# Kernel optimization log

Measured on AMD Instinct MI355X. Metric: run time of the kernel, lower is better.

## Reference

```python
import jax, jax.numpy as jnp
import numpy as np

M, K, N = 8192, 4096, 4096
ALPHA, BETA = 0.002, 0.0005


def setup_inputs() -> dict:
    key = jax.random.key(0)
    kx, kw, kb = jax.random.split(key, 3)
    # int8-range quantized activations and weights (stored as int32 for portability)
    x = jax.random.randint(kx, (M, K), -127, 127, dtype=jnp.int32)
    weight = jax.random.randint(kw, (N, K), -127, 127, dtype=jnp.int32)  # (out, in)
    bias = jax.random.randint(kb, (1, N), -(2**20), 2**20, dtype=jnp.int32)
    alpha = jnp.float32(ALPHA)
    beta = jnp.float32(BETA)
    return {"x": x, "weight": weight, "bias": bias, "alpha": alpha, "beta": beta}


def reference(x, weight, bias, alpha, beta):
    # int8 GEMM with int32 accumulation: acc[m, n] = sum_k x[m, k] * W[n, k]
    acc = jnp.matmul(x, weight.T, preferred_element_type=jnp.int32)  # [M, N] int32
    # CUTLASS-style epilogue: D = round(alpha * acc + beta * bias) -> int32
    y = alpha * acc.astype(jnp.float32) + beta * bias.astype(jnp.float32)
    return jnp.round(y).astype(jnp.int32)
```

## Files before the change

### kernel.cpp

```cpp
#include <hip/hip_runtime.h>
#include <hip/hip_bf16.h>
#include <stdint.h>

#define M_DIM 8192
#define N_DIM 4096
#define K_DIM 4096

#define BM 256
#define BN 256
#define BK 64
#define NT (K_DIM / BK)
#define DEPTH 4

typedef int v4i  __attribute__((ext_vector_type(4)));
typedef int v16i __attribute__((ext_vector_type(16)));

#define AS1C(p) ((const __attribute__((address_space(1))) void*)(p))
#define AS3(p)  ((__attribute__((address_space(3))) void*)(p))

__device__ __forceinline__ int pack4(int a, int b, int c, int d) {
  return (a & 0xff) | ((b & 0xff) << 8) | ((c & 0xff) << 16) | (d << 24);
}

__global__ void pack_both_kernel(const int* __restrict__ x, const int* __restrict__ w,
                                 char* __restrict__ A8, char* __restrict__ B8,
                                 int nA, int nTot) {
  int idx = blockIdx.x * blockDim.x + threadIdx.x;
  int stride = gridDim.x * blockDim.x;
  for (int i = idx; i < nTot; i += stride) {
    const int4* pin;
    int4* pout;
    if (i < nA) {
      pin  = (const int4*)x + 4 * (size_t)i;
      pout = (int4*)A8 + i;
    } else {
      int j = i - nA;
      pin  = (const int4*)w + 4 * (size_t)j;
      pout = (int4*)B8 + j;
    }
    int4 v0 = pin[0];
    int4 v1 = pin[1];
    int4 v2 = pin[2];
    int4 v3 = pin[3];
    int4 o;
    o.x = pack4(v0.x, v0.y, v0.z, v0.w);
    o.y = pack4(v1.x, v1.y, v1.z, v1.w);
    o.z = pack4(v2.x, v2.y, v2.z, v2.w);
    o.w = pack4(v3.x, v3.y, v3.z, v3.w);
    *pout = o;
  }
}

__global__ __launch_bounds__(512, 2) void gemm_i8_kernel(
    const char* __restrict__ A8, const char* __restrict__ B8,
    const int* __restrict__ bias, const float* __restrict__ alpha_p,
    const float* __restrict__ beta_p, int* __restrict__ out) {
  __shared__ alignas(16) char lds[DEPTH][BM * BK + BN * BK];

  const int tid  = threadIdx.x;
  const int lane = tid & 63;
  const int wave = tid >> 6;

  const int orig = blockIdx.x;
  const int swz  = (orig & 7) * (512 / 8) + (orig >> 3);
  const int bm   = (swz >> 4) * BM;
  const int bn   = (swz & 15) * BN;

  int aoff[2], boff[2], ldsoff[2];
#pragma unroll
  for (int i = 0; i < 2; ++i) {
    int linear = i * 8192 + tid * 16;
    int row = linear >> 6;
    int p   = (linear >> 4) & 3;
    int g   = p ^ ((row >> 1) & 3);
    ldsoff[i] = i * 8192 + wave * 1024;
    aoff[i] = (bm + row) * K_DIM + g * 16;
    boff[i] = (bn + row) * K_DIM + g * 16;
  }

#define STAGE_A(t)                                                                  \
  do {                                                                              \
    const char* ab_ = A8 + (t) * BK;                                                \
    char* base_ = &lds[(t) & (DEPTH - 1)][0];                                       \
    _Pragma("unroll") for (int i_ = 0; i_ < 2; ++i_)                                \
      __builtin_amdgcn_global_load_lds(AS1C(ab_ + aoff[i_]),                        \
                                       AS3(base_ + ldsoff[i_]), 16, 0, 0);          \
  } while (0)

#define STAGE_B(t)                                                                  \
  do {                                                                              \
    const char* bb_ = B8 + (t) * BK;                                                \
    char* base_ = &lds[(t) & (DEPTH - 1)][0];                                       \
    _Pragma("unroll") for (int i_ = 0; i_ < 2; ++i_)                                \
      __builtin_amdgcn_global_load_lds(AS1C(bb_ + boff[i_]),                        \
                                       AS3(base_ + 16384 + ldsoff[i_]), 16, 0, 0);  \
  } while (0)

  v16i acc[4][2];
#pragma unroll
  for (int i = 0; i < 4; ++i)
#pragma unroll
    for (int j = 0; j < 2; ++j)
#pragma unroll
      for (int r = 0; r < 16; ++r) acc[i][j][r] = 0;

  const int wr = wave >> 2;
  const int wc = wave & 3;
  const int l31   = lane & 31;
  const int khalf = lane >> 5;
  const int kxor  = (l31 >> 1) & 3;

#define COMPUTE_KS(t, ks)                                                           \
  do {                                                                              \
    const char* base_ = &lds[(t) & (DEPTH - 1)][0];                                 \
    const char* As_ = base_;                                                        \
    const char* Bs_ = base_ + 16384;                                                \
    const int coff_ = ((((ks) * 2 + khalf) ^ kxor) << 4);                           \
    v4i bf0 = *(const v4i*)(Bs_ + (wc * 64 + 0 * 32 + l31) * 64 + coff_);           \
    v4i bf1 = *(const v4i*)(Bs_ + (wc * 64 + 1 * 32 + l31) * 64 + coff_);           \
    v4i af0 = *(const v4i*)(As_ + (wr * 128 + 0 * 32 + l31) * 64 + coff_);          \
    v4i af1 = *(const v4i*)(As_ + (wr * 128 + 1 * 32 + l31) * 64 + coff_);          \
    v4i af2 = *(const v4i*)(As_ + (wr * 128 + 2 * 32 + l31) * 64 + coff_);          \
    v4i af3 = *(const v4i*)(As_ + (wr * 128 + 3 * 32 + l31) * 64 + coff_);          \
    asm volatile("s_waitcnt lgkmcnt(0)" ::: "memory");                              \
    __builtin_amdgcn_s_setprio(1);                                                  \
    acc[0][0] = __builtin_amdgcn_mfma_i32_32x32x32_i8(af0, bf0, acc[0][0], 0, 0, 0);\
    acc[1][0] = __builtin_amdgcn_mfma_i32_32x32x32_i8(af1, bf0, acc[1][0], 0, 0, 0);\
    acc[2][0] = __builtin_amdgcn_mfma_i32_32x32x32_i8(af2, bf0, acc[2][0], 0, 0, 0);\
    acc[3][0] = __builtin_amdgcn_mfma_i32_32x32x32_i8(af3, bf0, acc[3][0], 0, 0, 0);\
    acc[0][1] = __builtin_amdgcn_mfma_i32_32x32x32_i8(af0, bf1, acc[0][1], 0, 0, 0);\
    acc[1][1] = __builtin_amdgcn_mfma_i32_32x32x32_i8(af1, bf1, acc[1][1], 0, 0, 0);\
    acc[2][1] = __builtin_amdgcn_mfma_i32_32x32x32_i8(af2, bf1, acc[2][1], 0, 0, 0);\
    acc[3][1] = __builtin_amdgcn_mfma_i32_32x32x32_i8(af3, bf1, acc[3][1], 0, 0, 0);\
    __builtin_amdgcn_s_setprio(0);                                                  \
  } while (0)

  STAGE_A(0); STAGE_B(0);
  STAGE_A(1); STAGE_B(1);
  STAGE_A(2); STAGE_B(2);

  for (int t = 0; t < NT - 2; ++t) {
    asm volatile("s_waitcnt vmcnt(8) lgkmcnt(0)" ::: "memory");
    __builtin_amdgcn_s_barrier();
    if (t + 3 < NT) STAGE_A(t + 3);
    COMPUTE_KS(t, 0);
    __builtin_amdgcn_s_barrier();
    if (t + 3 < NT) STAGE_B(t + 3);
    COMPUTE_KS(t, 1);
  }
  asm volatile("s_waitcnt vmcnt(4) lgkmcnt(0)" ::: "memory");
  __builtin_amdgcn_s_barrier();
  COMPUTE_KS(NT - 2, 0);
  __builtin_amdgcn_s_barrier();
  COMPUTE_KS(NT - 2, 1);
  asm volatile("s_waitcnt vmcnt(0) lgkmcnt(0)" ::: "memory");
  __builtin_amdgcn_s_barrier();
  COMPUTE_KS(NT - 1, 0);
  __builtin_amdgcn_s_barrier();
  COMPUTE_KS(NT - 1, 1);

  const float alpha = *alpha_p;
  const float beta  = *beta_p;
  const int col0 = bn + wc * 64 + l31;
  float bb2[2];
#pragma unroll
  for (int nj = 0; nj < 2; ++nj) bb2[nj] = beta * (float)bias[col0 + nj * 32];

  const int rbase = bm + wr * 128 + 4 * khalf;
#pragma unroll
  for (int mi = 0; mi < 4; ++mi) {
#pragma unroll
    for (int q = 0; q < 4; ++q) {
#pragma unroll
      for (int rr = 0; rr < 4; ++rr) {
        int reg = q * 4 + rr;
        size_t rowoff = (size_t)(rbase + mi * 32 + rr + 8 * q) * N_DIM;
#pragma unroll
        for (int nj = 0; nj < 2; ++nj) {
          out[rowoff + col0 + nj * 32] =
              (int)rintf(fmaf(alpha, (float)acc[mi][nj][reg], bb2[nj]));
        }
      }
    }
  }
#undef STAGE_A
#undef STAGE_B
#undef COMPUTE_KS
}

__global__ void naive_kernel(const int* __restrict__ x, const int* __restrict__ w,
                             const int* __restrict__ bias,
                             const float* __restrict__ alpha_p,
                             const float* __restrict__ beta_p,
                             int* __restrict__ out) {
  size_t idx = (size_t)blockIdx.x * 256 + threadIdx.x;
  int m = (int)(idx / N_DIM);
  int n = (int)(idx % N_DIM);
  const int4* xr = (const int4*)(x + (size_t)m * K_DIM);
  const int4* wr = (const int4*)(w + (size_t)n * K_DIM);
  int acc = 0;
  for (int k = 0; k < K_DIM / 4; ++k) {
    int4 a = xr[k];
    int4 b = wr[k];
    acc += a.x * b.x + a.y * b.y + a.z * b.z + a.w * b.w;
  }
  out[idx] = (int)rintf(fmaf(*alpha_p, (float)acc, (*beta_p) * (float)bias[n]));
}

extern "C" void kernel_launch(void* const* d_in, const int* in_sizes, int n_in,
                              void* d_out, int out_size, void* d_ws, size_t ws_size,
                              hipStream_t stream) {
  const int*   x     = (const int*)d_in[0];
  const int*   w     = (const int*)d_in[1];
  const int*   bias  = (const int*)d_in[2];
  const float* alpha = (const float*)d_in[3];
  const float* beta  = (const float*)d_in[4];
  int* out = (int*)d_out;

  const size_t a8_bytes = (size_t)M_DIM * K_DIM;
  const size_t b8_bytes = (size_t)N_DIM * K_DIM;

  if (ws_size >= a8_bytes + b8_bytes) {
    char* A8 = (char*)d_ws;
    char* B8 = A8 + a8_bytes;
    const int nA = (int)(a8_bytes / 16);
    const int nTot = (int)((a8_bytes + b8_bytes) / 16);
    pack_both_kernel<<<2048, 256, 0, stream>>>(x, w, A8, B8, nA, nTot);
    const int nblk = (M_DIM / BM) * (N_DIM / BN);
    gemm_i8_kernel<<<nblk, 512, 0, stream>>>(A8, B8, bias, alpha, beta, out);
  } else {
    naive_kernel<<<(M_DIM * (size_t)N_DIM) / 256, 256, 0, stream>>>(x, w, bias, alpha, beta, out);
  }
}
```

Baseline: 202.6 us.

## Software-pipeline LDS fragment reads across K sub-steps and strengthen LDS swizzle

```diff
diff --git a/kernel.cpp b/kernel.cpp
--- a/kernel.cpp
+++ b/kernel.cpp
@@ -72,7 +72,7 @@
     int linear = i * 8192 + tid * 16;
     int row = linear >> 6;
     int p   = (linear >> 4) & 3;
-    int g   = p ^ ((row >> 1) & 3);
+    int g   = p ^ (((row >> 1) & 3) ^ ((row >> 3) & 3));
     ldsoff[i] = i * 8192 + wave * 1024;
     aoff[i] = (bm + row) * K_DIM + g * 16;
     boff[i] = (bn + row) * K_DIM + g * 16;
@@ -80,7 +80,7 @@
 
 #define STAGE_A(t)                                                                  \
   do {                                                                              \
-    const char* ab_ = A8 + (t) * BK;                                                \
+    const char* ab_ = A8 + (size_t)(t) * BK;                                        \
     char* base_ = &lds[(t) & (DEPTH - 1)][0];                                       \
     _Pragma("unroll") for (int i_ = 0; i_ < 2; ++i_)                                \
       __builtin_amdgcn_global_load_lds(AS1C(ab_ + aoff[i_]),                        \
@@ -89,7 +89,7 @@
 
 #define STAGE_B(t)                                                                  \
   do {                                                                              \
-    const char* bb_ = B8 + (t) * BK;                                                \
+    const char* bb_ = B8 + (size_t)(t) * BK;                                        \
     char* base_ = &lds[(t) & (DEPTH - 1)][0];                                       \
     _Pragma("unroll") for (int i_ = 0; i_ < 2; ++i_)                                \
       __builtin_amdgcn_global_load_lds(AS1C(bb_ + boff[i_]),                        \
@@ -108,56 +108,80 @@
   const int wc = wave & 3;
   const int l31   = lane & 31;
   const int khalf = lane >> 5;
-  const int kxor  = (l31 >> 1) & 3;
-
-#define COMPUTE_KS(t, ks)                                                           \
+  const int xswz = ((l31 >> 1) & 3) ^ ((l31 >> 3) & 3);
+  const int coff0 = ((0 * 2 + khalf) ^ xswz) << 4;
+  const int coff1 = ((1 * 2 + khalf) ^ xswz) << 4;
+
+  v4i af0a[4], bf0a[2], af0b[4], bf0b[2], af1[4], bf1[2];
+
+#define READ_KS0(S, t)                                                              \
   do {                                                                              \
     const char* base_ = &lds[(t) & (DEPTH - 1)][0];                                 \
-    const char* As_ = base_;                                                        \
-    const char* Bs_ = base_ + 16384;                                                \
-    const int coff_ = ((((ks) * 2 + khalf) ^ kxor) << 4);                           \
-    v4i bf0 = *(const v4i*)(Bs_ + (wc * 64 + 0 * 32 + l31) * 64 + coff_);           \
-    v4i bf1 = *(const v4i*)(Bs_ + (wc * 64 + 1 * 32 + l31) * 64 + coff_);           \
-    v4i af0 = *(const v4i*)(As_ + (wr * 128 + 0 * 32 + l31) * 64 + coff_);          \
-    v4i af1 = *(const v4i*)(As_ + (wr * 128 + 1 * 32 + l31) * 64 + coff_);          \
-    v4i af2 = *(const v4i*)(As_ + (wr * 128 + 2 * 32 + l31) * 64 + coff_);          \
-    v4i af3 = *(const v4i*)(As_ + (wr * 128 + 3 * 32 + l31) * 64 + coff_);          \
-    asm volatile("s_waitcnt lgkmcnt(0)" ::: "memory");                              \
+    _Pragma("unroll") for (int nj = 0; nj < 2; ++nj)                                \
+      bf0##S[nj] = *(const v4i*)(base_ + 16384 +                                    \
+                                 (wc * 64 + nj * 32 + l31) * 64 + coff0);           \
+    _Pragma("unroll") for (int mi = 0; mi < 4; ++mi)                                \
+      af0##S[mi] = *(const v4i*)(base_ + (wr * 128 + mi * 32 + l31) * 64 + coff0);  \
+  } while (0)
+
+#define READ_KS1(t)                                                                 \
+  do {                                                                              \
+    const char* base_ = &lds[(t) & (DEPTH - 1)][0];                                 \
+    _Pragma("unroll") for (int nj = 0; nj < 2; ++nj)                                \
+      bf1[nj] = *(const v4i*)(base_ + 16384 +                                       \
+                              (wc * 64 + nj * 32 + l31) * 64 + coff1);              \
+    _Pragma("unroll") for (int mi = 0; mi < 4; ++mi)                                \
+      af1[mi] = *(const v4i*)(base_ + (wr * 128 + mi * 32 + l31) * 64 + coff1);     \
+  } while (0)
+
+#define MFMA_KS0(S)                                                                 \
+  do {                                                                              \
     __builtin_amdgcn_s_setprio(1);                                                  \
-    acc[0][0] = __builtin_amdgcn_mfma_i32_32x32x32_i8(af0, bf0, acc[0][0], 0, 0, 0);\
-    acc[1][0] = __builtin_amdgcn_mfma_i32_32x32x32_i8(af1, bf0, acc[1][0], 0, 0, 0);\
-    acc[2][0] = __builtin_amdgcn_mfma_i32_32x32x32_i8(af2, bf0, acc[2][0], 0, 0, 0);\
-    acc[3][0] = __builtin_amdgcn_mfma_i32_32x32x32_i8(af3, bf0, acc[3][0], 0, 0, 0);\
-    acc[0][1] = __builtin_amdgcn_mfma_i32_32x32x32_i8(af0, bf1, acc[0][1], 0, 0, 0);\
-    acc[1][1] = __builtin_amdgcn_mfma_i32_32x32x32_i8(af1, bf1, acc[1][1], 0, 0, 0);\
-    acc[2][1] = __builtin_amdgcn_mfma_i32_32x32x32_i8(af2, bf1, acc[2][1], 0, 0, 0);\
-    acc[3][1] = __builtin_amdgcn_mfma_i32_32x32x32_i8(af3, bf1, acc[3][1], 0, 0, 0);\
+    _Pragma("unroll") for (int mi = 0; mi < 4; ++mi)                                \
+      _Pragma("unroll") for (int nj = 0; nj < 2; ++nj)                              \
+        acc[mi][nj] = __builtin_amdgcn_mfma_i32_32x32x32_i8(af0##S[mi], bf0##S[nj], \
+                                                            acc[mi][nj], 0, 0, 0); \
     __builtin_amdgcn_s_setprio(0);                                                  \
+  } while (0)
+
+#define MFMA_KS1()                                                                  \
+  do {                                                                              \
+    __builtin_amdgcn_s_setprio(1);                                                  \
+    _Pragma("unroll") for (int mi = 0; mi < 4; ++mi)                                \
+      _Pragma("unroll") for (int nj = 0; nj < 2; ++nj)                              \
+        acc[mi][nj] = __builtin_amdgcn_mfma_i32_32x32x32_i8(af1[mi], bf1[nj],       \
+                                                            acc[mi][nj], 0, 0, 0); \
+    __builtin_amdgcn_s_setprio(0);                                                  \
+  } while (0)
+
+#define TILE(t, C, N, STG, EV)                                                      \
+  do {                                                                              \
+    if (STG) STAGE_A((t) + 3);                                                      \
+    READ_KS1(t);                                                                    \
+    MFMA_KS0(C);                                                                    \
+    if (STG) STAGE_B((t) + 3);                                                      \
+    if ((t) + 1 < NT) READ_KS0(N, (t) + 1);                                         \
+    MFMA_KS1();                                                                     \
+    if ((EV) == 4) asm volatile("s_waitcnt vmcnt(4)" ::: "memory");                 \
+    if ((EV) == 0) asm volatile("s_waitcnt vmcnt(0)" ::: "memory");                 \
+    if ((EV) >= 0) __builtin_amdgcn_s_barrier();                                    \
   } while (0)
 
   STAGE_A(0); STAGE_B(0);
   STAGE_A(1); STAGE_B(1);
   STAGE_A(2); STAGE_B(2);
-
-  for (int t = 0; t < NT - 2; ++t) {
-    asm volatile("s_waitcnt vmcnt(8) lgkmcnt(0)" ::: "memory");
-    __builtin_amdgcn_s_barrier();
-    if (t + 3 < NT) STAGE_A(t + 3);
-    COMPUTE_KS(t, 0);
-    __builtin_amdgcn_s_barrier();
-    if (t + 3 < NT) STAGE_B(t + 3);
-    COMPUTE_KS(t, 1);
-  }
-  asm volatile("s_waitcnt vmcnt(4) lgkmcnt(0)" ::: "memory");
+  asm volatile("s_waitcnt vmcnt(4)" ::: "memory");
   __builtin_amdgcn_s_barrier();
-  COMPUTE_KS(NT - 2, 0);
-  __builtin_amdgcn_s_barrier();
-  COMPUTE_KS(NT - 2, 1);
-  asm volatile("s_waitcnt vmcnt(0) lgkmcnt(0)" ::: "memory");
-  __builtin_amdgcn_s_barrier();
-  COMPUTE_KS(NT - 1, 0);
-  __builtin_amdgcn_s_barrier();
-  COMPUTE_KS(NT - 1, 1);
+  READ_KS0(a, 0);
+
+  for (int t = 0; t < NT - 4; t += 2) {
+    TILE(t, a, b, true, 4);
+    TILE(t + 1, b, a, true, 4);
+  }
+  TILE(NT - 4, a, b, true, 4);
+  TILE(NT - 3, b, a, false, 0);
+  TILE(NT - 2, a, b, false, -1);
+  TILE(NT - 1, b, a, false, -1);
 
   const float alpha = *alpha_p;
   const float beta  = *beta_p;
@@ -185,7 +209,11 @@
   }
 #undef STAGE_A
 #undef STAGE_B
-#undef COMPUTE_KS
+#undef READ_KS0
+#undef READ_KS1
+#undef MFMA_KS0
+#undef MFMA_KS1
+#undef TILE
 }
 
 __global__ void naive_kernel(const int* __restrict__ x, const int* __restrict__ w,
```

Result: faster. 197.2 us (-2.7%).
